# Optimization experiments

Hardware: AMD Instinct MI355X
Metric: run time of the kernel (lower is better)

## Reference

```python
import jax, jax.numpy as jnp
import numpy as np

EPS = 1e-7


def _chamfer(p1, p2):
    # p1: (bs, N, 3), p2: (bs, M, 3)
    n1 = jnp.sum(p1 * p1, axis=-1)                    # (bs, N)
    n2 = jnp.sum(p2 * p2, axis=-1)                    # (bs, M)
    inner = jnp.einsum('bnd,bmd->bnm', p1, p2)        # (bs, N, M)
    d2 = n1[:, :, None] + n2[:, None, :] - 2.0 * inner
    d = jnp.sqrt(jnp.maximum(d2, 1e-12))              # L2 norm, as torch.norm(dim=3)
    # symmetric chamfer: sum of per-point nearest-neighbor distances, both ways
    cd = jnp.sum(jnp.min(d, axis=2)) + jnp.sum(jnp.min(d, axis=1))
    return cd


def setup_inputs() -> dict:
    key = jax.random.key(0)
    k1, k2, k3, k4, k5, k6, k7 = jax.random.split(key, 7)
    bs, K, N, M = 8, 1000, 4096, 4096
    return {
        'prob_pred': jax.random.uniform(k1, (bs, K), dtype=jnp.float32),
        'prob_target': jax.random.uniform(k2, (bs, K), dtype=jnp.float32),
        'x_diff_pred': jax.random.normal(k3, (bs, N, 3), dtype=jnp.float32),
        'x_diff_target': jax.random.normal(k4, (bs, M, 3), dtype=jnp.float32),
        'mu': jax.random.normal(k5, (K,), dtype=jnp.float32),
        'lower_bound': jax.random.uniform(k6, (K,), dtype=jnp.float32),
        'upper_bound': jax.random.uniform(k7, (K,), dtype=jnp.float32),
    }


def reference(prob_pred, prob_target, x_diff_pred, x_diff_target, mu, lower_bound, upper_bound):
    K = upper_bound.shape[0]
    # box-constraint term
    cr = jnp.abs(mu.reshape(lower_bound.shape)) - (lower_bound + upper_bound) / 2.0 + 1.0 / K
    CR = jnp.sum(jax.nn.relu(cr))
    # BCE with mean reduction (clamp like torch's internal log clamping)
    p = jnp.clip(prob_pred, EPS, 1.0 - EPS)
    BCE = -jnp.mean(prob_target * jnp.log(p) + (1.0 - prob_target) * jnp.log1p(-p))
    # chamfer distance
    CD = _chamfer(x_diff_pred, x_diff_target)
    return BCE + CD + CR
```

## Files before the change

### kernel.cpp

```cpp
#include <hip/hip_runtime.h>
#include <math.h>

#define EPSF 1e-7f
#define NP 4096

typedef __attribute__((ext_vector_type(8)))  short  short8;
typedef __attribute__((ext_vector_type(8)))  __bf16 bf16x8;
typedef __attribute__((ext_vector_type(16))) float  f32x16;

__device__ __forceinline__ unsigned short bf16_rn(float x) {
    unsigned int u = __float_as_uint(x);
    unsigned int r = u + 0x7FFFu + ((u >> 16) & 1u);
    return (unsigned short)(r >> 16);
}
__device__ __forceinline__ float bf16_to_f(unsigned short h) {
    return __uint_as_float(((unsigned int)h) << 16);
}

__device__ __forceinline__ void fold16(const f32x16& d, float& ra, float& rb) {
    ra = fminf(fminf(d[0],  d[1]),  ra);
    rb = fminf(fminf(d[2],  d[3]),  rb);
    ra = fminf(fminf(d[4],  d[5]),  ra);
    rb = fminf(fminf(d[6],  d[7]),  rb);
    ra = fminf(fminf(d[8],  d[9]),  ra);
    rb = fminf(fminf(d[10], d[11]), rb);
    ra = fminf(fminf(d[12], d[13]), ra);
    rb = fminf(fminf(d[14], d[15]), rb);
}

__device__ __forceinline__ bf16x8 make_qfrag(float x, float y, float z, int kg) {
    float m2x = -2.f * x, m2y = -2.f * y, m2z = -2.f * z;
    unsigned short xh = bf16_rn(m2x), yh = bf16_rn(m2y), zh = bf16_rn(m2z);
    unsigned short xl = bf16_rn(m2x - bf16_to_f(xh));
    unsigned short yl = bf16_rn(m2y - bf16_to_f(yh));
    unsigned short zl = bf16_rn(m2z - bf16_to_f(zh));
    short8 s;
    if (kg == 0)
        s = short8{(short)xh,(short)yh,(short)zh,(short)xl,(short)yl,(short)zl,(short)xh,(short)yh};
    else
        s = short8{(short)zh,(short)0x3F80,(short)0x3F80,0,0,0,0,0};
    return __builtin_bit_cast(bf16x8, s);
}

__global__ __launch_bounds__(512, 2) void chamfer_fused(
    const float* __restrict__ pred, const float* __restrict__ targ,
    float* __restrict__ parts)
{
    const int tid  = threadIdx.x;
    const int lane = tid & 63, w = tid >> 6, kg = lane >> 5;
    const int half = w >> 2;
    const int strip = blockIdx.x;
    const int combo = blockIdx.y;
    const int dir = combo >> 3, b = combo & 7;

    __shared__ char  panel[131072];
    __shared__ float redbuf[512];
    __shared__ float red4[4];

    const float* Q = (dir ? targ : pred) + (size_t)b * NP * 3;
    const int qA = strip * 256 + (w & 3) * 64 + (lane & 31);
    const int qB = qA + 32;
    const float ax = Q[qA * 3], ay = Q[qA * 3 + 1], az = Q[qA * 3 + 2];
    const float bx = Q[qB * 3], by = Q[qB * 3 + 1], bz = Q[qB * 3 + 2];
    const bf16x8 fragA = make_qfrag(ax, ay, az, kg);
    const bf16x8 fragB = make_qfrag(bx, by, bz, kg);
    const float n1A = fmaf(ax, ax, fmaf(ay, ay, az * az));
    const float n1B = fmaf(bx, bx, fmaf(by, by, bz * bz));

    const float* D = (dir ? pred : targ) + (size_t)b * NP * 3;
#pragma unroll
    for (int i = 0; i < 8; ++i) {
        const int pt = i * 512 + tid;
        const float* dp = D + (size_t)pt * 3;
        float x = dp[0], y = dp[1], z = dp[2];
        float n2 = fmaf(x, x, fmaf(y, y, z * z));
        unsigned short xh = bf16_rn(x), yh = bf16_rn(y), zh = bf16_rn(z);
        unsigned short xl = bf16_rn(x - bf16_to_f(xh));
        unsigned short yl = bf16_rn(y - bf16_to_f(yh));
        unsigned short zl = bf16_rn(z - bf16_to_f(zh));
        unsigned short nh = bf16_rn(n2);
        unsigned short nl = bf16_rn(n2 - bf16_to_f(nh));
        short8 k0 = short8{(short)xh,(short)yh,(short)zh,
                           (short)xh,(short)yh,(short)zh,
                           (short)xl,(short)yl};
        short8 k1 = short8{(short)zl,(short)nh,(short)nl,0,0,0,0,0};
        char* base = panel + (pt >> 5) * 1024 + (pt & 31) * 16;
        *(short8*)base         = k0;
        *(short8*)(base + 512) = k1;
    }
    __syncthreads();

    float rA0 = 3.4e38f, rA1 = 3.4e38f, rB0 = 3.4e38f, rB1 = 3.4e38f;
    const f32x16 zero = {0.f};
    const char* abase = panel + (size_t)half * 65536 + kg * 512 + (lane & 31) * 16;

    bf16x8 af = *(const bf16x8*)(abase);
#pragma unroll 4
    for (int t = 0; t < 63; ++t) {
        bf16x8 afn = *(const bf16x8*)(abase + (t + 1) * 1024);
        f32x16 d0 = __builtin_amdgcn_mfma_f32_32x32x16_bf16(af, fragA, zero, 0, 0, 0);
        f32x16 d1 = __builtin_amdgcn_mfma_f32_32x32x16_bf16(af, fragB, zero, 0, 0, 0);
        fold16(d0, rA0, rA1);
        fold16(d1, rB0, rB1);
        af = afn;
    }
    {
        f32x16 d0 = __builtin_amdgcn_mfma_f32_32x32x16_bf16(af, fragA, zero, 0, 0, 0);
        f32x16 d1 = __builtin_amdgcn_mfma_f32_32x32x16_bf16(af, fragB, zero, 0, 0, 0);
        fold16(d0, rA0, rA1);
        fold16(d1, rB0, rB1);
    }

    float rA = fminf(rA0, rA1);  rA = fminf(rA, __shfl_xor(rA, 32));
    float rB = fminf(rB0, rB1);  rB = fminf(rB, __shfl_xor(rB, 32));
    float val = (lane < 32) ? (rA + n1A) : (rB + n1B);
    __syncthreads();
    redbuf[half * 256 + (w & 3) * 64 + lane] = val;
    __syncthreads();

    if (tid < 256) {
        float m = fminf(redbuf[tid], redbuf[256 + tid]);
        float dist = sqrtf(fmaxf(m, 1e-12f));
        for (int off = 32; off; off >>= 1) dist += __shfl_xor(dist, off);
        if ((tid & 63) == 0) red4[tid >> 6] = dist;
    }
    __syncthreads();
    if (tid == 0)
        parts[blockIdx.y * 16 + blockIdx.x] = red4[0] + red4[1] + red4[2] + red4[3];
}

__global__ __launch_bounds__(256) void finalize_kernel(
    const float* __restrict__ parts,
    const float* __restrict__ prob_pred, const float* __restrict__ prob_target,
    const float* __restrict__ mu, const float* __restrict__ lb,
    const float* __restrict__ ub,
    float* __restrict__ out, int nprob, int K)
{
    const int tid = threadIdx.x;

    float bce = 0.f;
    const float pmax = 1.0f - EPSF;
    for (int i = tid; i < nprob; i += 256) {
        float p = prob_pred[i];
        p = fminf(fmaxf(p, EPSF), pmax);
        float t = prob_target[i];
        bce += t * logf(p) + (1.0f - t) * log1pf(-p);
    }

    float cr = 0.f;
    const float invK = 1.0f / (float)K;
    for (int i = tid; i < K; i += 256) {
        float c = fabsf(mu[i]) - 0.5f * (lb[i] + ub[i]) + invK;
        cr += fmaxf(c, 0.f);
    }

    float v1 = parts[tid] + cr;
    float v2 = bce;
    for (int off = 32; off; off >>= 1) {
        v1 += __shfl_xor(v1, off);
        v2 += __shfl_xor(v2, off);
    }
    __shared__ float s1[4], s2[4];
    if ((tid & 63) == 0) { s1[tid >> 6] = v1; s2[tid >> 6] = v2; }
    __syncthreads();
    if (tid == 0) {
        float V1 = s1[0] + s1[1] + s1[2] + s1[3];
        float V2 = s2[0] + s2[1] + s2[2] + s2[3];
        out[0] = V1 - V2 / (float)nprob;
    }
}

extern "C" void kernel_launch(void* const* d_in, const int* in_sizes, int n_in,
                              void* d_out, int out_size, void* d_ws, size_t ws_size,
                              hipStream_t stream) {
    const float* prob_pred   = (const float*)d_in[0];
    const float* prob_target = (const float*)d_in[1];
    const float* x_pred      = (const float*)d_in[2];
    const float* x_target    = (const float*)d_in[3];
    const float* mu          = (const float*)d_in[4];
    const float* lb          = (const float*)d_in[5];
    const float* ub          = (const float*)d_in[6];
    float* out   = (float*)d_out;
    float* parts = (float*)d_ws;

    const int K     = in_sizes[4];
    const int nprob = in_sizes[0];

    dim3 grid(16, 16);
    chamfer_fused<<<grid, 512, 0, stream>>>(x_pred, x_target, parts);
    finalize_kernel<<<1, 256, 0, stream>>>(parts, prob_pred, prob_target,
                                           mu, lb, ub, out, nprob, K);
}
```

Before: 28.93 us.

## Split chamfer database across grid z with separate min-reduce kernel

The chamfer kernel now splits each batch's database points into four quarters along a new grid dimension. It uses 256-thread blocks with a 32KB LDS panel instead of 512 threads with 128KB, giving four times as many blocks and higher occupancy. Partial per-query minima go to workspace, and a new reduce kernel takes the min across quarters, applies sqrt and sums. The per-MFMA fold is replaced with elementwise vector min accumulators that are folded only once at the end. In exchange it adds a third kernel launch, a global round-trip for the partial minima, and more accumulator registers.

```diff
diff --git a/kernel.cpp b/kernel.cpp
--- a/kernel.cpp
+++ b/kernel.cpp
@@ -17,15 +17,16 @@
     return __uint_as_float(((unsigned int)h) << 16);
 }
 
-__device__ __forceinline__ void fold16(const f32x16& d, float& ra, float& rb) {
-    ra = fminf(fminf(d[0],  d[1]),  ra);
-    rb = fminf(fminf(d[2],  d[3]),  rb);
-    ra = fminf(fminf(d[4],  d[5]),  ra);
-    rb = fminf(fminf(d[6],  d[7]),  rb);
-    ra = fminf(fminf(d[8],  d[9]),  ra);
-    rb = fminf(fminf(d[10], d[11]), rb);
-    ra = fminf(fminf(d[12], d[13]), ra);
-    rb = fminf(fminf(d[14], d[15]), rb);
+__device__ __forceinline__ void vmin16(f32x16& acc, const f32x16& d) {
+#pragma unroll
+    for (int i = 0; i < 16; ++i) acc[i] = fminf(acc[i], d[i]);
+}
+__device__ __forceinline__ float fold_scalar(const f32x16& a) {
+    float m0 = fminf(fminf(a[0], a[1]),  fminf(a[2], a[3]));
+    float m1 = fminf(fminf(a[4], a[5]),  fminf(a[6], a[7]));
+    float m2 = fminf(fminf(a[8], a[9]),  fminf(a[10], a[11]));
+    float m3 = fminf(fminf(a[12], a[13]), fminf(a[14], a[15]));
+    return fminf(fminf(m0, m1), fminf(m2, m3));
 }
 
 __device__ __forceinline__ bf16x8 make_qfrag(float x, float y, float z, int kg) {
@@ -42,23 +43,21 @@
     return __builtin_bit_cast(bf16x8, s);
 }
 
-__global__ __launch_bounds__(512, 2) void chamfer_fused(
+__global__ __launch_bounds__(256, 4) void chamfer_q(
     const float* __restrict__ pred, const float* __restrict__ targ,
-    float* __restrict__ parts)
+    float* __restrict__ ws)
 {
     const int tid  = threadIdx.x;
     const int lane = tid & 63, w = tid >> 6, kg = lane >> 5;
-    const int half = w >> 2;
-    const int strip = blockIdx.x;
-    const int combo = blockIdx.y;
+    const int strip   = blockIdx.x;
+    const int combo   = blockIdx.y;
+    const int quarter = blockIdx.z;
     const int dir = combo >> 3, b = combo & 7;
 
-    __shared__ char  panel[131072];
-    __shared__ float redbuf[512];
-    __shared__ float red4[4];
+    __shared__ char panel[32768];
 
     const float* Q = (dir ? targ : pred) + (size_t)b * NP * 3;
-    const int qA = strip * 256 + (w & 3) * 64 + (lane & 31);
+    const int qA = strip * 256 + w * 64 + (lane & 31);
     const int qB = qA + 32;
     const float ax = Q[qA * 3], ay = Q[qA * 3 + 1], az = Q[qA * 3 + 2];
     const float bx = Q[qB * 3], by = Q[qB * 3 + 1], bz = Q[qB * 3 + 2];
@@ -67,10 +66,10 @@
     const float n1A = fmaf(ax, ax, fmaf(ay, ay, az * az));
     const float n1B = fmaf(bx, bx, fmaf(by, by, bz * bz));
 
-    const float* D = (dir ? pred : targ) + (size_t)b * NP * 3;
+    const float* D = (dir ? pred : targ) + ((size_t)b * NP + quarter * 1024) * 3;
 #pragma unroll
-    for (int i = 0; i < 8; ++i) {
-        const int pt = i * 512 + tid;
+    for (int i = 0; i < 4; ++i) {
+        const int pt = i * 256 + tid;
         const float* dp = D + (size_t)pt * 3;
         float x = dp[0], y = dp[1], z = dp[2];
         float n2 = fmaf(x, x, fmaf(y, y, z * z));
@@ -90,43 +89,49 @@
     }
     __syncthreads();
 
-    float rA0 = 3.4e38f, rA1 = 3.4e38f, rB0 = 3.4e38f, rB1 = 3.4e38f;
+    f32x16 accA, accB;
+#pragma unroll
+    for (int i = 0; i < 16; ++i) { accA[i] = 3.4e38f; accB[i] = 3.4e38f; }
     const f32x16 zero = {0.f};
-    const char* abase = panel + (size_t)half * 65536 + kg * 512 + (lane & 31) * 16;
-
-    bf16x8 af = *(const bf16x8*)(abase);
+    const char* abase = panel + kg * 512 + (lane & 31) * 16;
+
+    bf16x8 af = *(const bf16x8*)abase;
 #pragma unroll 4
-    for (int t = 0; t < 63; ++t) {
+    for (int t = 0; t < 31; ++t) {
         bf16x8 afn = *(const bf16x8*)(abase + (t + 1) * 1024);
         f32x16 d0 = __builtin_amdgcn_mfma_f32_32x32x16_bf16(af, fragA, zero, 0, 0, 0);
         f32x16 d1 = __builtin_amdgcn_mfma_f32_32x32x16_bf16(af, fragB, zero, 0, 0, 0);
-        fold16(d0, rA0, rA1);
-        fold16(d1, rB0, rB1);
+        vmin16(accA, d0);
+        vmin16(accB, d1);
         af = afn;
     }
     {
         f32x16 d0 = __builtin_amdgcn_mfma_f32_32x32x16_bf16(af, fragA, zero, 0, 0, 0);
         f32x16 d1 = __builtin_amdgcn_mfma_f32_32x32x16_bf16(af, fragB, zero, 0, 0, 0);
-        fold16(d0, rA0, rA1);
-        fold16(d1, rB0, rB1);
-    }
-
-    float rA = fminf(rA0, rA1);  rA = fminf(rA, __shfl_xor(rA, 32));
-    float rB = fminf(rB0, rB1);  rB = fminf(rB, __shfl_xor(rB, 32));
+        vmin16(accA, d0);
+        vmin16(accB, d1);
+    }
+
+    float rA = fold_scalar(accA);  rA = fminf(rA, __shfl_xor(rA, 32));
+    float rB = fold_scalar(accB);  rB = fminf(rB, __shfl_xor(rB, 32));
     float val = (lane < 32) ? (rA + n1A) : (rB + n1B);
+    const int q = strip * 256 + w * 64 + lane;
+    ws[(size_t)((combo << 12) + q) * 4 + quarter] = val;
+}
+
+__global__ __launch_bounds__(256) void reduce_q(
+    const float* __restrict__ ws, float* __restrict__ parts)
+{
+    const int tid = threadIdx.x;
+    const int g = blockIdx.x * 256 + tid;
+    float4 v = ((const float4*)ws)[g];
+    float m = fminf(fminf(v.x, v.y), fminf(v.z, v.w));
+    float dist = sqrtf(fmaxf(m, 1e-12f));
+    for (int off = 32; off; off >>= 1) dist += __shfl_xor(dist, off);
+    __shared__ float red[4];
+    if ((tid & 63) == 0) red[tid >> 6] = dist;
     __syncthreads();
-    redbuf[half * 256 + (w & 3) * 64 + lane] = val;
-    __syncthreads();
-
-    if (tid < 256) {
-        float m = fminf(redbuf[tid], redbuf[256 + tid]);
-        float dist = sqrtf(fmaxf(m, 1e-12f));
-        for (int off = 32; off; off >>= 1) dist += __shfl_xor(dist, off);
-        if ((tid & 63) == 0) red4[tid >> 6] = dist;
-    }
-    __syncthreads();
-    if (tid == 0)
-        parts[blockIdx.y * 16 + blockIdx.x] = red4[0] + red4[1] + red4[2] + red4[3];
+    if (tid == 0) parts[blockIdx.x] = red[0] + red[1] + red[2] + red[3];
 }
 
 __global__ __launch_bounds__(256) void finalize_kernel(
@@ -181,13 +186,15 @@
     const float* lb          = (const float*)d_in[5];
     const float* ub          = (const float*)d_in[6];
     float* out   = (float*)d_out;
-    float* parts = (float*)d_ws;
+    float* ws    = (float*)d_ws;
+    float* parts = ws + 65536 * 4;
 
     const int K     = in_sizes[4];
     const int nprob = in_sizes[0];
 
-    dim3 grid(16, 16);
-    chamfer_fused<<<grid, 512, 0, stream>>>(x_pred, x_target, parts);
+    dim3 grid(16, 16, 4);
+    chamfer_q<<<grid, 256, 0, stream>>>(x_pred, x_target, ws);
+    reduce_q<<<256, 256, 0, stream>>>(ws, parts);
     finalize_kernel<<<1, 256, 0, stream>>>(parts, prob_pred, prob_target,
                                            mu, lb, ub, out, nprob, K);
 }
```

After: 30.19 us. +4.3%, slower.

## Fuse chamfer and finalize kernels via cooperative grid sync

Applied to the files above, without the earlier changes.

Merges the chamfer kernel and the single-block finalize kernel into one cooperative launch, with a grid-wide sync before block 0 computes the BCE, box term and final sum. The MFMA loop is also reworked so each iteration issues the next pair of MFMAs before folding the previous results, software-pipelining the min-reduction behind the matrix ops. This removes a second kernel launch and its gap, but adds the cost of a cooperative launch and grid barrier, and drops the occupancy hint from launch bounds.

```diff
diff --git a/kernel.cpp b/kernel.cpp
--- a/kernel.cpp
+++ b/kernel.cpp
@@ -1,5 +1,8 @@
 #include <hip/hip_runtime.h>
+#include <hip/hip_cooperative_groups.h>
 #include <math.h>
+
+namespace cg = cooperative_groups;
 
 #define EPSF 1e-7f
 #define NP 4096
@@ -42,20 +45,25 @@
     return __builtin_bit_cast(bf16x8, s);
 }
 
-__global__ __launch_bounds__(512, 2) void chamfer_fused(
+__global__ __launch_bounds__(512) void vae_fused(
     const float* __restrict__ pred, const float* __restrict__ targ,
-    float* __restrict__ parts)
+    const float* __restrict__ prob_pred, const float* __restrict__ prob_target,
+    const float* __restrict__ mu, const float* __restrict__ lb,
+    const float* __restrict__ ub, float* __restrict__ out,
+    float* __restrict__ parts, int nprob, int K)
 {
+    __shared__ char  panel[131072];
+    __shared__ float redbuf[512];
+    __shared__ float red4[4];
+    __shared__ float s1[8], s2[8];
+
     const int tid  = threadIdx.x;
     const int lane = tid & 63, w = tid >> 6, kg = lane >> 5;
     const int half = w >> 2;
-    const int strip = blockIdx.x;
-    const int combo = blockIdx.y;
+    const int bid  = blockIdx.x;
+    const int strip = bid & 15;
+    const int combo = bid >> 4;
     const int dir = combo >> 3, b = combo & 7;
-
-    __shared__ char  panel[131072];
-    __shared__ float redbuf[512];
-    __shared__ float red4[4];
 
     const float* Q = (dir ? targ : pred) + (size_t)b * NP * 3;
     const int qA = strip * 256 + (w & 3) * 64 + (lane & 31);
@@ -94,22 +102,20 @@
     const f32x16 zero = {0.f};
     const char* abase = panel + (size_t)half * 65536 + kg * 512 + (lane & 31) * 16;
 
-    bf16x8 af = *(const bf16x8*)(abase);
-#pragma unroll 4
-    for (int t = 0; t < 63; ++t) {
-        bf16x8 afn = *(const bf16x8*)(abase + (t + 1) * 1024);
-        f32x16 d0 = __builtin_amdgcn_mfma_f32_32x32x16_bf16(af, fragA, zero, 0, 0, 0);
-        f32x16 d1 = __builtin_amdgcn_mfma_f32_32x32x16_bf16(af, fragB, zero, 0, 0, 0);
-        fold16(d0, rA0, rA1);
-        fold16(d1, rB0, rB1);
-        af = afn;
-    }
-    {
-        f32x16 d0 = __builtin_amdgcn_mfma_f32_32x32x16_bf16(af, fragA, zero, 0, 0, 0);
-        f32x16 d1 = __builtin_amdgcn_mfma_f32_32x32x16_bf16(af, fragB, zero, 0, 0, 0);
-        fold16(d0, rA0, rA1);
-        fold16(d1, rB0, rB1);
-    }
+    bf16x8 af = *(const bf16x8*)abase;
+    f32x16 c0 = __builtin_amdgcn_mfma_f32_32x32x16_bf16(af, fragA, zero, 0, 0, 0);
+    f32x16 c1 = __builtin_amdgcn_mfma_f32_32x32x16_bf16(af, fragB, zero, 0, 0, 0);
+#pragma unroll 3
+    for (int t = 1; t < 64; ++t) {
+        bf16x8 af2 = *(const bf16x8*)(abase + t * 1024);
+        f32x16 n0 = __builtin_amdgcn_mfma_f32_32x32x16_bf16(af2, fragA, zero, 0, 0, 0);
+        f32x16 n1 = __builtin_amdgcn_mfma_f32_32x32x16_bf16(af2, fragB, zero, 0, 0, 0);
+        fold16(c0, rA0, rA1);
+        fold16(c1, rB0, rB1);
+        c0 = n0; c1 = n1;
+    }
+    fold16(c0, rA0, rA1);
+    fold16(c1, rB0, rB1);
 
     float rA = fminf(rA0, rA1);  rA = fminf(rA, __shfl_xor(rA, 32));
     float rB = fminf(rB0, rB1);  rB = fminf(rB, __shfl_xor(rB, 32));
@@ -126,21 +132,17 @@
     }
     __syncthreads();
     if (tid == 0)
-        parts[blockIdx.y * 16 + blockIdx.x] = red4[0] + red4[1] + red4[2] + red4[3];
-}
-
-__global__ __launch_bounds__(256) void finalize_kernel(
-    const float* __restrict__ parts,
-    const float* __restrict__ prob_pred, const float* __restrict__ prob_target,
-    const float* __restrict__ mu, const float* __restrict__ lb,
-    const float* __restrict__ ub,
-    float* __restrict__ out, int nprob, int K)
-{
-    const int tid = threadIdx.x;
+        parts[bid] = red4[0] + red4[1] + red4[2] + red4[3];
+
+    __threadfence();
+    cg::this_grid().sync();
+
+    if (bid != 0) return;
+    __threadfence();
 
     float bce = 0.f;
     const float pmax = 1.0f - EPSF;
-    for (int i = tid; i < nprob; i += 256) {
+    for (int i = tid; i < nprob; i += 512) {
         float p = prob_pred[i];
         p = fminf(fmaxf(p, EPSF), pmax);
         float t = prob_target[i];
@@ -149,23 +151,23 @@
 
     float cr = 0.f;
     const float invK = 1.0f / (float)K;
-    for (int i = tid; i < K; i += 256) {
+    for (int i = tid; i < K; i += 512) {
         float c = fabsf(mu[i]) - 0.5f * (lb[i] + ub[i]) + invK;
         cr += fmaxf(c, 0.f);
     }
 
-    float v1 = parts[tid] + cr;
+    float v1 = (tid < 256 ? parts[tid] : 0.f) + cr;
     float v2 = bce;
     for (int off = 32; off; off >>= 1) {
         v1 += __shfl_xor(v1, off);
         v2 += __shfl_xor(v2, off);
     }
-    __shared__ float s1[4], s2[4];
-    if ((tid & 63) == 0) { s1[tid >> 6] = v1; s2[tid >> 6] = v2; }
+    if (lane == 0) { s1[w] = v1; s2[w] = v2; }
     __syncthreads();
     if (tid == 0) {
-        float V1 = s1[0] + s1[1] + s1[2] + s1[3];
-        float V2 = s2[0] + s2[1] + s2[2] + s2[3];
+        float V1 = 0.f, V2 = 0.f;
+#pragma unroll
+        for (int i = 0; i < 8; ++i) { V1 += s1[i]; V2 += s2[i]; }
         out[0] = V1 - V2 / (float)nprob;
     }
 }
@@ -183,11 +185,16 @@
     float* out   = (float*)d_out;
     float* parts = (float*)d_ws;
 
-    const int K     = in_sizes[4];
-    const int nprob = in_sizes[0];
-
-    dim3 grid(16, 16);
-    chamfer_fused<<<grid, 512, 0, stream>>>(x_pred, x_target, parts);
-    finalize_kernel<<<1, 256, 0, stream>>>(parts, prob_pred, prob_target,
-                                           mu, lb, ub, out, nprob, K);
-}
+    int nprob = in_sizes[0];
+    int K     = in_sizes[4];
+
+    void* args[] = {
+        (void*)&x_pred, (void*)&x_target,
+        (void*)&prob_pred, (void*)&prob_target,
+        (void*)&mu, (void*)&lb, (void*)&ub,
+        (void*)&out, (void*)&parts,
+        (void*)&nprob, (void*)&K
+    };
+    hipLaunchCooperativeKernel((const void*)vae_fused,
+                               dim3(256), dim3(512), args, 0, stream);
+}
```

Result: slower. 87.85 us (+203.7%).
